# Performance work log

Measured on AMD Instinct MI355X. Metric: run time of the kernel, lower is better.

The kernel has to match this reference:

```python
import jax, jax.numpy as jnp
import numpy as np

EPS = 1e-5

def _bn(x, gamma, beta):
    # x: [B, N, C]; training-mode BatchNorm1d over (B, N)
    mu = jnp.mean(x, axis=(0, 1))
    var = jnp.var(x, axis=(0, 1))
    return (x - mu) * jax.lax.rsqrt(var + EPS) * gamma + beta


def setup_inputs() -> dict:
    key = jax.random.key(0)
    ks = jax.random.split(key, 32)
    B, N = 16, 8192
    enc_dim, mem_dim = 1024, 1024
    feat_dim = enc_dim + mem_dim  # 2048
    n_points = 2048
    s = 0.02
    d = {
        'partial': jax.random.normal(ks[0], (B, N, 3), jnp.float32),
        # first_conv: Conv1d(3,128,1) + BN(128) + ReLU + Conv1d(128,256,1)
        'W1': jax.random.normal(ks[1], (128, 3), jnp.float32) * s,
        'b1': jnp.zeros((128,), jnp.float32),
        'g1': jnp.ones((128,), jnp.float32),
        'be1': jnp.zeros((128,), jnp.float32),
        'W2': jax.random.normal(ks[2], (256, 128), jnp.float32) * s,
        'b2': jnp.zeros((256,), jnp.float32),
        # second_conv: Conv1d(512,512,1) + BN(512) + ReLU + Conv1d(512,enc_dim,1)
        'W3': jax.random.normal(ks[3], (512, 512), jnp.float32) * s,
        'b3': jnp.zeros((512,), jnp.float32),
        'g2': jnp.ones((512,), jnp.float32),
        'be2': jnp.zeros((512,), jnp.float32),
        'W4': jax.random.normal(ks[4], (enc_dim, 512), jnp.float32) * s,
        'b4': jnp.zeros((enc_dim,), jnp.float32),
        # MemoryModule gates: Linear(enc_dim, mem_dim) x4 + memory param
        'Wf': jax.random.normal(ks[5], (mem_dim, enc_dim), jnp.float32) * s,
        'bf': jnp.zeros((mem_dim,), jnp.float32),
        'Wi': jax.random.normal(ks[6], (mem_dim, enc_dim), jnp.float32) * s,
        'bi': jnp.zeros((mem_dim,), jnp.float32),
        'Wo': jax.random.normal(ks[7], (mem_dim, enc_dim), jnp.float32) * s,
        'bo': jnp.zeros((mem_dim,), jnp.float32),
        'Wc': jax.random.normal(ks[8], (mem_dim, enc_dim), jnp.float32) * s,
        'bc': jnp.zeros((mem_dim,), jnp.float32),
        'mem': jax.random.normal(ks[9], (1, mem_dim), jnp.float32),
        # Decoder MLP: feat_dim->2048->2048->2048->3*n_points
        'D1w': jax.random.normal(ks[10], (2048, feat_dim), jnp.float32) * s,
        'D1b': jnp.zeros((2048,), jnp.float32),
        'D2w': jax.random.normal(ks[11], (2048, 2048), jnp.float32) * s,
        'D2b': jnp.zeros((2048,), jnp.float32),
        'D3w': jax.random.normal(ks[12], (2048, 2048), jnp.float32) * s,
        'D3b': jnp.zeros((2048,), jnp.float32),
        'D4w': jax.random.normal(ks[13], (3 * n_points, 2048), jnp.float32) * s,
        'D4b': jnp.zeros((3 * n_points,), jnp.float32),
    }
    return d


def reference(partial, W1, b1, g1, be1, W2, b2, W3, b3, g2, be2, W4, b4,
              Wf, bf, Wi, bi, Wo, bo, Wc, bc, mem,
              D1w, D1b, D2w, D2b, D3w, D3b, D4w, D4b):
    B, N, _ = partial.shape
    # --- Encoder first_conv (pointwise convs == per-point linear) ---
    f = jnp.einsum('bnc,dc->bnd', partial, W1) + b1          # [B,N,128]
    f = jax.nn.relu(_bn(f, g1, be1))
    f = jnp.einsum('bnc,dc->bnd', f, W2) + b2                # [B,N,256]
    fg = jnp.max(f, axis=1, keepdims=True)                   # [B,1,256]
    f = jnp.concatenate([jnp.broadcast_to(fg, (B, N, 256)), f], axis=-1)  # [B,N,512]
    # --- second_conv ---
    f = jnp.einsum('bnc,dc->bnd', f, W3) + b3                # [B,N,512]
    f = jax.nn.relu(_bn(f, g2, be2))
    f = jnp.einsum('bnc,dc->bnd', f, W4) + b4                # [B,N,enc_dim]
    feat_global = jnp.max(f, axis=1)                         # [B,enc_dim]
    # --- MemoryModule (flag=False: memory not updated) ---
    fgate = jax.nn.sigmoid(feat_global @ Wf.T + bf)
    igate = jax.nn.sigmoid(feat_global @ Wi.T + bi)
    ogate = jax.nn.sigmoid(feat_global @ Wo.T + bo)
    cand = jnp.tanh(feat_global @ Wc.T + bc)
    mem_b = jnp.broadcast_to(mem, fgate.shape)
    h = ogate * jnp.tanh(fgate * mem_b + igate * cand)       # [B,mem_dim]
    feat = jnp.concatenate([feat_global, h], axis=1)         # [B,feat_dim]
    # --- Decoder MLP ---
    z = jax.nn.relu(feat @ D1w.T + D1b)
    z = jax.nn.relu(z @ D2w.T + D2b)
    z = jax.nn.relu(z @ D3w.T + D3b)
    z = z @ D4w.T + D4b                                      # [B, 3*n_points]
    return z.reshape(B, -1, 3)
```

## Files before the change

kernel.cpp:

```cpp
#include <hip/hip_runtime.h>
#include <hip/hip_bf16.h>

typedef __bf16 v8bf __attribute__((ext_vector_type(8)));
typedef float  v4f  __attribute__((ext_vector_type(4)));

#define NPTS (16*8192)
#define RPB  8192

__device__ __forceinline__ unsigned fenc(float x){
    unsigned u = __float_as_uint(x);
    return (u & 0x80000000u) ? ~u : (u | 0x80000000u);
}
__device__ __forceinline__ float fdec(unsigned u){
    return __uint_as_float((u & 0x80000000u) ? (u ^ 0x80000000u) : ~u);
}

__device__ __forceinline__ v8bf bn_relu8(v8bf v, float4 s0, float4 s1, float4 h0, float4 h1){
    v8bf r;
    r[0] = (__bf16)fmaxf(fmaf((float)v[0], s0.x, h0.x), 0.f);
    r[1] = (__bf16)fmaxf(fmaf((float)v[1], s0.y, h0.y), 0.f);
    r[2] = (__bf16)fmaxf(fmaf((float)v[2], s0.z, h0.z), 0.f);
    r[3] = (__bf16)fmaxf(fmaf((float)v[3], s0.w, h0.w), 0.f);
    r[4] = (__bf16)fmaxf(fmaf((float)v[4], s1.x, h1.x), 0.f);
    r[5] = (__bf16)fmaxf(fmaf((float)v[5], s1.y, h1.y), 0.f);
    r[6] = (__bf16)fmaxf(fmaf((float)v[6], s1.z, h1.z), 0.f);
    r[7] = (__bf16)fmaxf(fmaf((float)v[7], s1.w, h1.w), 0.f);
    return r;
}

__global__ __launch_bounds__(256) void stats1_k(const float* __restrict__ P,
        const float* __restrict__ W1, const float* __restrict__ b1,
        float* __restrict__ gsum, float* __restrict__ gsumsq)
{
    int tid = threadIdx.x;
    int c = tid & 127, half = tid >> 7;
    float w0 = W1[c*3+0], w1 = W1[c*3+1], w2 = W1[c*3+2], bb = b1[c];
    float s = 0.f, s2 = 0.f;
    int base = blockIdx.x * 512 + half;
    for (int i = 0; i < 256; ++i) {
        int p = base + i*2;
        float x = P[p*3+0], y = P[p*3+1], z = P[p*3+2];
        float v = fmaf(w0,x, fmaf(w1,y, fmaf(w2,z, bb)));
        s += v; s2 = fmaf(v,v,s2);
    }
    __shared__ float ls[256], lq[256];
    ls[tid] = s; lq[tid] = s2;
    __syncthreads();
    if (half == 0) {
        atomicAdd(&gsum[c],   s  + ls[tid+128]);
        atomicAdd(&gsumsq[c], s2 + lq[tid+128]);
    }
}

__global__ void finalize_k(const float* __restrict__ gsum, const float* __restrict__ gsumsq,
        const float* __restrict__ gamma, const float* __restrict__ beta,
        float* __restrict__ scale, float* __restrict__ shift, int C, float invn)
{
    int c = blockIdx.x*blockDim.x + threadIdx.x;
    if (c >= C) return;
    float m   = gsum[c]*invn;
    float var = fmaxf(gsumsq[c]*invn - m*m, 0.f);
    float rs  = rsqrtf(var + 1e-5f);
    float sc  = gamma[c]*rs;
    scale[c] = sc;
    shift[c] = beta[c] - m*sc;
}

__global__ __launch_bounds__(256) void apply1_k(const float* __restrict__ P,
        const float* __restrict__ W1, const float* __restrict__ b1,
        const float* __restrict__ sc, const float* __restrict__ sh,
        __bf16* __restrict__ out)
{
    int tid = threadIdx.x;
    int c = tid & 127, ph = tid >> 7;
    float w0 = W1[c*3+0], w1 = W1[c*3+1], w2 = W1[c*3+2], bb = b1[c];
    float a = sc[c], b_ = sh[c];
    int base = blockIdx.x * 16 + ph;
    #pragma unroll
    for (int i = 0; i < 8; ++i) {
        int p = base + i*2;
        float x = P[p*3+0], y = P[p*3+1], z = P[p*3+2];
        float v = fmaf(w0,x, fmaf(w1,y, fmaf(w2,z, bb)));
        v = fmaxf(fmaf(v, a, b_), 0.f);
        out[(size_t)p*128 + c] = (__bf16)v;
    }
}

__global__ void cvt_k(const float* __restrict__ src, __bf16* __restrict__ dst,
                      int rows, int cols, int sstride, int coff)
{
    int i = blockIdx.x*256 + threadIdx.x;
    if (i >= rows*cols) return;
    int r = i / cols, c = i - r*cols;
    dst[i] = (__bf16)src[(size_t)r*sstride + coff + c];
}

template<bool STORE, bool DOMAX, int LOGNB>
__global__ __launch_bounds__(256, 2) void gemm_k(
        const __bf16* __restrict__ A, const __bf16* __restrict__ Bw,
        int K, int Nw,
        const float* __restrict__ bias, int bias_bstride,
        __bf16* __restrict__ Cout, unsigned* __restrict__ maxenc)
{
    __shared__ __bf16 As[128*64];
    __shared__ __bf16 Bs[128*64];
    const int tid  = threadIdx.x;
    const int lane = tid & 63;
    const int wave = tid >> 6;
    const int wr = wave >> 1, wc = wave & 1;
    const int nwg   = (int)gridDim.x;
    const int chunk = nwg >> 3;
    const int bi    = (int)blockIdx.x;
    const int li    = (bi & 7) * chunk + (bi >> 3);
    const int m0    = (li >> LOGNB) * 128;
    const int n0    = (li & ((1 << LOGNB) - 1)) * 128;
    const int srow = tid >> 3, sslot = tid & 7;

    v4f acc[4][4];
    #pragma unroll
    for (int i=0;i<4;i++)
      #pragma unroll
      for (int j=0;j<4;j++) acc[i][j] = (v4f)(0.0f);

    v8bf ra[4], rb[4];
    #pragma unroll
    for (int i=0;i<4;i++){
        int r = i*32 + srow;
        ra[i] = *(const v8bf*)(A  + (size_t)(m0+r)*K + sslot*8);
        rb[i] = *(const v8bf*)(Bw + (size_t)(n0+r)*K + sslot*8);
    }

    for (int k0 = 0; k0 < K; k0 += 64) {
        __syncthreads();
        #pragma unroll
        for (int i=0;i<4;i++){
            int r = i*32 + srow;
            int p = sslot ^ (r & 7);
            *(v8bf*)(&As[r*64 + p*8]) = ra[i];
            *(v8bf*)(&Bs[r*64 + p*8]) = rb[i];
        }
        __syncthreads();
        if (k0 + 64 < K) {
            #pragma unroll
            for (int i=0;i<4;i++){
                int r = i*32 + srow;
                ra[i] = *(const v8bf*)(A  + (size_t)(m0+r)*K + (k0+64) + sslot*8);
                rb[i] = *(const v8bf*)(Bw + (size_t)(n0+r)*K + (k0+64) + sslot*8);
            }
        }
        #pragma unroll
        for (int kk = 0; kk < 2; ++kk) {
            v8bf af[4], bfr[4];
            #pragma unroll
            for (int i=0;i<4;i++){
                int arow = wr*64 + i*16 + (lane & 15);
                int slog = kk*4 + (lane >> 4);
                af[i]  = *(const v8bf*)(&As[arow*64 + ((slog ^ (arow & 7))<<3)]);
                int brow = wc*64 + i*16 + (lane & 15);
                bfr[i] = *(const v8bf*)(&Bs[brow*64 + ((slog ^ (brow & 7))<<3)]);
            }
            #pragma unroll
            for (int i=0;i<4;i++)
              #pragma unroll
              for (int j=0;j<4;j++)
                acc[i][j] = __builtin_amdgcn_mfma_f32_16x16x32_bf16(af[i], bfr[j], acc[i][j], 0,0,0);
        }
    }

    const int b = m0 / RPB;
    const float* brow_ = bias + (size_t)b * bias_bstride;
    float colmax[4];
    #pragma unroll
    for (int j=0;j<4;j++) colmax[j] = -3.402823466e38f;

    #pragma unroll
    for (int i=0;i<4;i++){
        int rbase = m0 + wr*64 + i*16 + ((lane>>4)<<2);
        #pragma unroll
        for (int j=0;j<4;j++){
            int col = n0 + wc*64 + j*16 + (lane & 15);
            float bv = brow_[col];
            #pragma unroll
            for (int q=0;q<4;q++){
                float v = acc[i][j][q] + bv;
                if constexpr (STORE) Cout[(size_t)(rbase+q)*Nw + col] = (__bf16)v;
                if constexpr (DOMAX) colmax[j] = fmaxf(colmax[j], v);
            }
        }
    }
    if constexpr (DOMAX) {
        #pragma unroll
        for (int j=0;j<4;j++){
            float v = colmax[j];
            v = fmaxf(v, __shfl_xor(v, 16));
            v = fmaxf(v, __shfl_xor(v, 32));
            if (lane < 16) {
                int col = n0 + wc*64 + j*16 + lane;
                atomicMax(&maxenc[(size_t)b*Nw + col], fenc(v));
            }
        }
    }
}

template<bool STORE, bool DOMAX, bool STATS, bool BNA, int LOGNB>
__global__ __launch_bounds__(512, 2) void gemm8_k(
        const __bf16* __restrict__ A, const __bf16* __restrict__ Bw,
        int K, int Nw,
        const float* __restrict__ bias, int bias_bstride,
        __bf16* __restrict__ Cout, unsigned* __restrict__ maxenc,
        float* __restrict__ gsum, float* __restrict__ gsq,
        const float* __restrict__ scA, const float* __restrict__ shA)
{
    __shared__ __bf16 lds[2][2][256*64];
    __shared__ float bnbuf[2][512];

    const int tid  = threadIdx.x;
    const int lane = tid & 63;
    const int wave = tid >> 6;
    const int wr = wave >> 2, wc = wave & 3;
    const int nwg   = (int)gridDim.x;
    const int chunk = nwg >> 3;
    const int bi    = (int)blockIdx.x;
    const int li    = (bi & 7) * chunk + (bi >> 3);
    const int m0    = (li >> LOGNB) * 256;
    const int n0    = (li & ((1 << LOGNB) - 1)) * 256;
    const int srow = tid >> 3;
    const int slot = tid & 7;

    if constexpr (BNA) {
        for (int c = tid; c < K; c += 512) {
            bnbuf[0][c] = scA[c];
            bnbuf[1][c] = shA[c];
        }
    }

    v4f acc[8][4];
    #pragma unroll
    for (int i=0;i<8;i++)
      #pragma unroll
      for (int j=0;j<4;j++) acc[i][j] = (v4f)(0.0f);

    v8bf ga[4], gb[4];
    auto issue = [&](int kb){
        #pragma unroll
        for (int p=0;p<4;p++){
            int r = p*64 + srow;
            ga[p] = *(const v8bf*)(A  + (size_t)(m0+r)*K + kb + slot*8);
            gb[p] = *(const v8bf*)(Bw + (size_t)(n0+r)*K + kb + slot*8);
        }
    };
    auto wr_lds = [&](int buf, int kb){
        float4 s0{}, s1{}, h0{}, h1{};
        if constexpr (BNA) {
            int kk = kb + slot*8;
            s0 = *(const float4*)&bnbuf[0][kk];
            s1 = *(const float4*)&bnbuf[0][kk+4];
            h0 = *(const float4*)&bnbuf[1][kk];
            h1 = *(const float4*)&bnbuf[1][kk+4];
        }
        #pragma unroll
        for (int p=0;p<4;p++){
            int r = p*64 + srow;
            int sl = slot ^ (r & 7);
            v8bf va = ga[p];
            if constexpr (BNA) va = bn_relu8(va, s0, s1, h0, h1);
            *(v8bf*)(&lds[buf][0][r*64 + sl*8]) = va;
            *(v8bf*)(&lds[buf][1][r*64 + sl*8]) = gb[p];
        }
    };

    if constexpr (BNA) __syncthreads();
    issue(0);
    wr_lds(0, 0);
    issue(64);
    __syncthreads();

    const int nt = K >> 6;
    for (int t = 0; t < nt; ++t) {
        const __bf16* as_ = &lds[t & 1][0][0];
        const __bf16* bs_ = &lds[t & 1][1][0];
        v8bf bfr[4][2];
        #pragma unroll
        for (int ph = 0; ph < 4; ++ph) {
            v8bf af[2][2];
            if (ph == 0) {
                #pragma unroll
                for (int nf=0;nf<4;nf++)
                  #pragma unroll
                  for (int kk=0;kk<2;kk++){
                    int brow = wc*64 + nf*16 + (lane & 15);
                    int sg = kk*4 + (lane >> 4);
                    bfr[nf][kk] = *(const v8bf*)(bs_ + brow*64 + ((sg ^ (brow & 7))<<3));
                  }
            }
            #pragma unroll
            for (int i=0;i<2;i++)
              #pragma unroll
              for (int kk=0;kk<2;kk++){
                int arow = wr*128 + (ph*2+i)*16 + (lane & 15);
                int sg = kk*4 + (lane >> 4);
                af[i][kk] = *(const v8bf*)(as_ + arow*64 + ((sg ^ (arow & 7))<<3));
              }
            __builtin_amdgcn_s_barrier();
            asm volatile("s_waitcnt lgkmcnt(0)" ::: "memory");
            __builtin_amdgcn_sched_barrier(0);
            __builtin_amdgcn_s_setprio(1);
            #pragma unroll
            for (int i=0;i<2;i++)
              #pragma unroll
              for (int nf=0;nf<4;nf++)
                acc[ph*2+i][nf] = __builtin_amdgcn_mfma_f32_16x16x32_bf16(af[i][0], bfr[nf][0], acc[ph*2+i][nf], 0,0,0);
            #pragma unroll
            for (int i=0;i<2;i++)
              #pragma unroll
              for (int nf=0;nf<4;nf++)
                acc[ph*2+i][nf] = __builtin_amdgcn_mfma_f32_16x16x32_bf16(af[i][1], bfr[nf][1], acc[ph*2+i][nf], 0,0,0);
            __builtin_amdgcn_s_setprio(0);
            if (ph < 3) {
                __builtin_amdgcn_s_barrier();
            } else {
                __syncthreads();
                if (t + 1 < nt) wr_lds((t+1) & 1, (t+1) << 6);
                if (t + 2 < nt) issue((t+2) << 6);
                __syncthreads();
            }
        }
    }

    const int b = m0 / RPB;
    const float* brow_ = bias + (size_t)b * bias_bstride;
    float colmax[4], csum[4], csq[4];
    #pragma unroll
    for (int j=0;j<4;j++){ colmax[j] = -3.402823466e38f; csum[j]=0.f; csq[j]=0.f; }

    #pragma unroll
    for (int i=0;i<8;i++){
        int rbase = m0 + wr*128 + i*16 + ((lane>>4)<<2);
        #pragma unroll
        for (int j=0;j<4;j++){
            int col = n0 + wc*64 + j*16 + (lane & 15);
            float bv = brow_[col];
            #pragma unroll
            for (int q=0;q<4;q++){
                float v = acc[i][j][q] + bv;
                if constexpr (STORE) Cout[(size_t)(rbase+q)*Nw + col] = (__bf16)v;
                if constexpr (DOMAX) colmax[j] = fmaxf(colmax[j], v);
                if constexpr (STATS) { csum[j] += v; csq[j] = fmaf(v,v,csq[j]); }
            }
        }
    }
    if constexpr (DOMAX) {
        #pragma unroll
        for (int j=0;j<4;j++){
            float v = colmax[j];
            v = fmaxf(v, __shfl_xor(v, 16));
            v = fmaxf(v, __shfl_xor(v, 32));
            if (lane < 16) {
                int col = n0 + wc*64 + j*16 + lane;
                atomicMax(&maxenc[(size_t)b*Nw + col], fenc(v));
            }
        }
    }
    if constexpr (STATS) {
        float* lst = (float*)&lds[0][0][0];
        #pragma unroll
        for (int j=0;j<4;j++){
            float s = csum[j], q = csq[j];
            s += __shfl_xor(s, 16); s += __shfl_xor(s, 32);
            q += __shfl_xor(q, 16); q += __shfl_xor(q, 32);
            if (lane < 16) {
                int c = wc*64 + j*16 + lane;
                lst[(wr*2+0)*256 + c] = s;
                lst[(wr*2+1)*256 + c] = q;
            }
        }
        __syncthreads();
        if (tid < 256) {
            float s = lst[0*256 + tid] + lst[2*256 + tid];
            float q = lst[1*256 + tid] + lst[3*256 + tid];
            atomicAdd(&gsum[n0 + tid], s);
            atomicAdd(&gsq [n0 + tid], q);
        }
    }
}

__global__ __launch_bounds__(256) void bias3_k(const unsigned* __restrict__ fge,
        const float* __restrict__ W3, const float* __restrict__ b3,
        float* __restrict__ bias3)
{
    int b = blockIdx.x, tid = threadIdx.x;
    __shared__ float fg[256];
    fg[tid] = fdec(fge[b*256 + tid]);
    __syncthreads();
    for (int d = tid; d < 512; d += 256) {
        const float* wrow = W3 + (size_t)d*512;
        float s = b3[d];
        for (int c = 0; c < 256; c += 4) {
            s = fmaf(fg[c+0], wrow[c+0], s);
            s = fmaf(fg[c+1], wrow[c+1], s);
            s = fmaf(fg[c+2], wrow[c+2], s);
            s = fmaf(fg[c+3], wrow[c+3], s);
        }
        bias3[b*512 + d] = s;
    }
}

__global__ void decode_k(const unsigned* __restrict__ enc, float* __restrict__ feat)
{
    int i = blockIdx.x*256 + threadIdx.x;
    int b = i >> 10, c = i & 1023;
    feat[(size_t)b*2048 + c] = fdec(enc[i]);
}

__global__ __launch_bounds__(256) void gates_k(
        const float* __restrict__ Wf, const float* __restrict__ bfv,
        const float* __restrict__ Wi, const float* __restrict__ biv,
        const float* __restrict__ Wo, const float* __restrict__ bov,
        const float* __restrict__ Wc, const float* __restrict__ bcv,
        const float* __restrict__ memv, float* __restrict__ feat)
{
    int tid = threadIdx.x;
    int b = tid & 15;
    int j = blockIdx.x*16 + (tid >> 4);
    const float* x  = feat + (size_t)b*2048;
    const float* rf = Wf + (size_t)j*1024;
    const float* ri = Wi + (size_t)j*1024;
    const float* ro = Wo + (size_t)j*1024;
    const float* rc = Wc + (size_t)j*1024;
    float sf = bfv[j], si = biv[j], so = bov[j], scn = bcv[j];
    for (int c = 0; c < 1024; c += 4) {
        float4 xv = *(const float4*)(x + c);
        float4 a  = *(const float4*)(rf + c);
        sf = fmaf(xv.x,a.x, fmaf(xv.y,a.y, fmaf(xv.z,a.z, fmaf(xv.w,a.w, sf))));
        float4 bq = *(const float4*)(ri + c);
        si = fmaf(xv.x,bq.x, fmaf(xv.y,bq.y, fmaf(xv.z,bq.z, fmaf(xv.w,bq.w, si))));
        float4 cq = *(const float4*)(ro + c);
        so = fmaf(xv.x,cq.x, fmaf(xv.y,cq.y, fmaf(xv.z,cq.z, fmaf(xv.w,cq.w, so))));
        float4 dq = *(const float4*)(rc + c);
        scn= fmaf(xv.x,dq.x, fmaf(xv.y,dq.y, fmaf(xv.z,dq.z, fmaf(xv.w,dq.w, scn))));
    }
    float fg = 1.f/(1.f + expf(-sf));
    float ig = 1.f/(1.f + expf(-si));
    float og = 1.f/(1.f + expf(-so));
    float cd = tanhf(scn);
    float h  = og * tanhf(fmaf(fg, memv[j], ig*cd));
    feat[(size_t)b*2048 + 1024 + j] = h;
}

template<bool RELU>
__global__ __launch_bounds__(256) void dec_k(const float* __restrict__ in,
        const float* __restrict__ W, const float* __restrict__ bias,
        float* __restrict__ out, int N)
{
    __shared__ float xin[2048];
    int tid = threadIdx.x;
    int b    = (blockIdx.x*4) / N;
    int col0 = (blockIdx.x*4) % N;
    for (int k = tid; k < 2048; k += 256) xin[k] = in[(size_t)b*2048 + k];
    __syncthreads();
    int lane = tid & 63;
    int col  = col0 + (tid >> 6);
    const float* wrow = W + (size_t)col*2048;
    float s = 0.f;
    for (int k = lane*4; k < 2048; k += 256) {
        float4 wv = *(const float4*)(wrow + k);
        float4 xv = *(const float4*)(&xin[k]);
        s = fmaf(wv.x,xv.x, fmaf(wv.y,xv.y, fmaf(wv.z,xv.z, fmaf(wv.w,xv.w, s))));
    }
    #pragma unroll
    for (int off = 32; off; off >>= 1) s += __shfl_xor(s, off);
    if (lane == 0) {
        s += bias[col];
        if (RELU) s = fmaxf(s, 0.f);
        out[(size_t)b*N + col] = s;
    }
}

extern "C" void kernel_launch(void* const* d_in, const int* in_sizes, int n_in,
                              void* d_out, int out_size, void* d_ws, size_t ws_size,
                              hipStream_t stream)
{
    (void)in_sizes; (void)n_in; (void)out_size; (void)ws_size;
    const float* partial = (const float*)d_in[0];
    const float* W1 = (const float*)d_in[1];
    const float* b1 = (const float*)d_in[2];
    const float* g1 = (const float*)d_in[3];
    const float* be1= (const float*)d_in[4];
    const float* W2 = (const float*)d_in[5];
    const float* b2 = (const float*)d_in[6];
    const float* W3 = (const float*)d_in[7];
    const float* b3 = (const float*)d_in[8];
    const float* g2 = (const float*)d_in[9];
    const float* be2= (const float*)d_in[10];
    const float* W4 = (const float*)d_in[11];
    const float* b4 = (const float*)d_in[12];
    const float* Wf = (const float*)d_in[13];
    const float* bfv= (const float*)d_in[14];
    const float* Wi = (const float*)d_in[15];
    const float* biv= (const float*)d_in[16];
    const float* Wo = (const float*)d_in[17];
    const float* bov= (const float*)d_in[18];
    const float* Wc = (const float*)d_in[19];
    const float* bcv= (const float*)d_in[20];
    const float* memv=(const float*)d_in[21];
    const float* D1w= (const float*)d_in[22];
    const float* D1b= (const float*)d_in[23];
    const float* D2w= (const float*)d_in[24];
    const float* D2b= (const float*)d_in[25];
    const float* D3w= (const float*)d_in[26];
    const float* D3b= (const float*)d_in[27];
    const float* D4w= (const float*)d_in[28];
    const float* D4b= (const float*)d_in[29];

    char* w = (char*)d_ws;
    size_t off = 0;
    auto alloc = [&](size_t bytes) -> void* {
        void* p = w + off; off += (bytes + 255) & ~(size_t)255; return p;
    };
    __bf16* y1bn = (__bf16*)alloc((size_t)NPTS*128*2);
    __bf16* f2   = (__bf16*)alloc((size_t)NPTS*256*2);
    __bf16* y3   = (__bf16*)alloc((size_t)NPTS*512*2);
    __bf16* W2b  = (__bf16*)alloc(256*128*2);
    __bf16* W3bb = (__bf16*)alloc(512*256*2);
    __bf16* W4b  = (__bf16*)alloc(1024*512*2);
    char* accbase = (char*)(w + off);
    float* gsum1    = (float*)alloc(128*4);
    float* gsumsq1  = (float*)alloc(128*4);
    float* gsum3    = (float*)alloc(512*4);
    float* gsumsq3  = (float*)alloc(512*4);
    unsigned* fg_enc    = (unsigned*)alloc(16*256*4);
    unsigned* featg_enc = (unsigned*)alloc(16*1024*4);
    size_t accbytes = (size_t)((w + off) - accbase);
    float* scale1 = (float*)alloc(128*4);
    float* shift1 = (float*)alloc(128*4);
    float* scale3 = (float*)alloc(512*4);
    float* shift3 = (float*)alloc(512*4);
    float* bias3  = (float*)alloc(16*512*4);
    float* feat   = (float*)alloc(16*2048*4);
    float* z1     = (float*)alloc(16*2048*4);
    float* z2     = (float*)alloc(16*2048*4);
    float* z3     = (float*)alloc(16*2048*4);

    hipMemsetAsync(accbase, 0, accbytes, stream);

    cvt_k<<<dim3(128), 256, 0, stream>>>(W2, W2b, 256, 128, 128, 0);
    cvt_k<<<dim3(512), 256, 0, stream>>>(W3, W3bb, 512, 256, 512, 256);
    cvt_k<<<dim3(2048),256, 0, stream>>>(W4, W4b, 1024, 512, 512, 0);

    stats1_k<<<dim3(256), 256, 0, stream>>>(partial, W1, b1, gsum1, gsumsq1);
    finalize_k<<<dim3(1), 128, 0, stream>>>(gsum1, gsumsq1, g1, be1, scale1, shift1, 128, 1.f/NPTS);
    apply1_k<<<dim3(8192), 256, 0, stream>>>(partial, W1, b1, scale1, shift1, y1bn);

    gemm_k<true,true,1><<<dim3(2048), 256, 0, stream>>>(
        y1bn, W2b, 128, 256, b2, 0, f2, fg_enc);

    bias3_k<<<dim3(16), 256, 0, stream>>>(fg_enc, W3, b3, bias3);

    gemm8_k<true,false,true,false,1><<<dim3(1024), 512, 0, stream>>>(
        f2, W3bb, 256, 512, bias3, 512, y3, nullptr, gsum3, gsumsq3, nullptr, nullptr);

    finalize_k<<<dim3(2), 256, 0, stream>>>(gsum3, gsumsq3, g2, be2, scale3, shift3, 512, 1.f/NPTS);

    gemm8_k<false,true,false,true,2><<<dim3(2048), 512, 0, stream>>>(
        y3, W4b, 512, 1024, b4, 0, nullptr, featg_enc, nullptr, nullptr, scale3, shift3);

    decode_k<<<dim3(64), 256, 0, stream>>>(featg_enc, feat);
    gates_k<<<dim3(64), 256, 0, stream>>>(Wf,bfv, Wi,biv, Wo,bov, Wc,bcv, memv, feat);

    dec_k<true ><<<dim3(8192),  256, 0, stream>>>(feat, D1w, D1b, z1, 2048);
    dec_k<true ><<<dim3(8192),  256, 0, stream>>>(z1,   D2w, D2b, z2, 2048);
    dec_k<true ><<<dim3(8192),  256, 0, stream>>>(z2,   D3w, D3b, z3, 2048);
    dec_k<false><<<dim3(24576), 256, 0, stream>>>(z3,   D4w, D4b, (float*)d_out, 6144);
}
```

Measured before the change: 574.2 us.

## Shrink GEMM M-tile with simpler single-buffer loop and batch decoder across all rows

The large-tile GEMM kernel is replaced by one using 128x256 tiles, a single LDS buffer with register prefetch, and BN+ReLU applied to A directly from global scale and shift arrays. Grid sizes double to match the smaller tile. The decoder GEMV kernel now keeps all 16 batch rows in LDS, so each weight row is read once instead of 16 times. This cuts decoder weight traffic sharply. The GEMM loses its double buffering and explicit MFMA scheduling, which may hurt its throughput.

```diff
diff --git a/kernel.cpp b/kernel.cpp
--- a/kernel.cpp
+++ b/kernel.cpp
@@ -203,7 +203,7 @@
 }
 
 template<bool STORE, bool DOMAX, bool STATS, bool BNA, int LOGNB>
-__global__ __launch_bounds__(512, 2) void gemm8_k(
+__global__ __launch_bounds__(512, 2) void gemmw_k(
         const __bf16* __restrict__ A, const __bf16* __restrict__ Bw,
         int K, int Nw,
         const float* __restrict__ bias, int bias_bstride,
@@ -211,9 +211,9 @@
         float* __restrict__ gsum, float* __restrict__ gsq,
         const float* __restrict__ scA, const float* __restrict__ shA)
 {
-    __shared__ __bf16 lds[2][2][256*64];
-    __shared__ float bnbuf[2][512];
-
+    __shared__ __bf16 As[128*64];
+    __shared__ __bf16 Bs[256*64];
+    __shared__ float lstat[2][2][256];
     const int tid  = threadIdx.x;
     const int lane = tid & 63;
     const int wave = tid >> 6;
@@ -222,108 +222,75 @@
     const int chunk = nwg >> 3;
     const int bi    = (int)blockIdx.x;
     const int li    = (bi & 7) * chunk + (bi >> 3);
-    const int m0    = (li >> LOGNB) * 256;
+    const int m0    = (li >> LOGNB) * 128;
     const int n0    = (li & ((1 << LOGNB) - 1)) * 256;
     const int srow = tid >> 3;
     const int slot = tid & 7;
 
-    if constexpr (BNA) {
-        for (int c = tid; c < K; c += 512) {
-            bnbuf[0][c] = scA[c];
-            bnbuf[1][c] = shA[c];
-        }
-    }
-
-    v4f acc[8][4];
-    #pragma unroll
-    for (int i=0;i<8;i++)
+    v4f acc[4][4];
+    #pragma unroll
+    for (int i=0;i<4;i++)
       #pragma unroll
       for (int j=0;j<4;j++) acc[i][j] = (v4f)(0.0f);
 
-    v8bf ga[4], gb[4];
-    auto issue = [&](int kb){
-        #pragma unroll
-        for (int p=0;p<4;p++){
-            int r = p*64 + srow;
-            ga[p] = *(const v8bf*)(A  + (size_t)(m0+r)*K + kb + slot*8);
-            gb[p] = *(const v8bf*)(Bw + (size_t)(n0+r)*K + kb + slot*8);
-        }
-    };
-    auto wr_lds = [&](int buf, int kb){
+    v8bf ra[2], rb[4];
+    auto loadAB = [&](int kb){
         float4 s0{}, s1{}, h0{}, h1{};
         if constexpr (BNA) {
             int kk = kb + slot*8;
-            s0 = *(const float4*)&bnbuf[0][kk];
-            s1 = *(const float4*)&bnbuf[0][kk+4];
-            h0 = *(const float4*)&bnbuf[1][kk];
-            h1 = *(const float4*)&bnbuf[1][kk+4];
-        }
-        #pragma unroll
-        for (int p=0;p<4;p++){
-            int r = p*64 + srow;
-            int sl = slot ^ (r & 7);
-            v8bf va = ga[p];
-            if constexpr (BNA) va = bn_relu8(va, s0, s1, h0, h1);
-            *(v8bf*)(&lds[buf][0][r*64 + sl*8]) = va;
-            *(v8bf*)(&lds[buf][1][r*64 + sl*8]) = gb[p];
+            s0 = *(const float4*)(scA + kk);
+            s1 = *(const float4*)(scA + kk + 4);
+            h0 = *(const float4*)(shA + kk);
+            h1 = *(const float4*)(shA + kk + 4);
+        }
+        #pragma unroll
+        for (int i=0;i<2;i++){
+            int r = i*64 + srow;
+            v8bf v = *(const v8bf*)(A + (size_t)(m0+r)*K + kb + slot*8);
+            if constexpr (BNA) v = bn_relu8(v, s0, s1, h0, h1);
+            ra[i] = v;
+        }
+        #pragma unroll
+        for (int i=0;i<4;i++){
+            int r = i*64 + srow;
+            rb[i] = *(const v8bf*)(Bw + (size_t)(n0+r)*K + kb + slot*8);
         }
     };
 
-    if constexpr (BNA) __syncthreads();
-    issue(0);
-    wr_lds(0, 0);
-    issue(64);
-    __syncthreads();
-
-    const int nt = K >> 6;
-    for (int t = 0; t < nt; ++t) {
-        const __bf16* as_ = &lds[t & 1][0][0];
-        const __bf16* bs_ = &lds[t & 1][1][0];
-        v8bf bfr[4][2];
-        #pragma unroll
-        for (int ph = 0; ph < 4; ++ph) {
-            v8bf af[2][2];
-            if (ph == 0) {
-                #pragma unroll
-                for (int nf=0;nf<4;nf++)
-                  #pragma unroll
-                  for (int kk=0;kk<2;kk++){
-                    int brow = wc*64 + nf*16 + (lane & 15);
-                    int sg = kk*4 + (lane >> 4);
-                    bfr[nf][kk] = *(const v8bf*)(bs_ + brow*64 + ((sg ^ (brow & 7))<<3));
-                  }
-            }
-            #pragma unroll
-            for (int i=0;i<2;i++)
+    loadAB(0);
+
+    for (int k0 = 0; k0 < K; k0 += 64) {
+        __syncthreads();
+        #pragma unroll
+        for (int i=0;i<2;i++){
+            int r = i*64 + srow;
+            int p = slot ^ (r & 7);
+            *(v8bf*)(&As[r*64 + p*8]) = ra[i];
+        }
+        #pragma unroll
+        for (int i=0;i<4;i++){
+            int r = i*64 + srow;
+            int p = slot ^ (r & 7);
+            *(v8bf*)(&Bs[r*64 + p*8]) = rb[i];
+        }
+        __syncthreads();
+        if (k0 + 64 < K) loadAB(k0 + 64);
+        #pragma unroll
+        for (int kk = 0; kk < 2; ++kk) {
+            v8bf af[4], bfr[4];
+            #pragma unroll
+            for (int i=0;i<4;i++){
+                int arow = wr*64 + i*16 + (lane & 15);
+                int sg = kk*4 + (lane >> 4);
+                af[i]  = *(const v8bf*)(&As[arow*64 + ((sg ^ (arow & 7))<<3)]);
+                int brow = wc*64 + i*16 + (lane & 15);
+                bfr[i] = *(const v8bf*)(&Bs[brow*64 + ((sg ^ (brow & 7))<<3)]);
+            }
+            #pragma unroll
+            for (int i=0;i<4;i++)
               #pragma unroll
-              for (int kk=0;kk<2;kk++){
-                int arow = wr*128 + (ph*2+i)*16 + (lane & 15);
-                int sg = kk*4 + (lane >> 4);
-                af[i][kk] = *(const v8bf*)(as_ + arow*64 + ((sg ^ (arow & 7))<<3));
-              }
-            __builtin_amdgcn_s_barrier();
-            asm volatile("s_waitcnt lgkmcnt(0)" ::: "memory");
-            __builtin_amdgcn_sched_barrier(0);
-            __builtin_amdgcn_s_setprio(1);
-            #pragma unroll
-            for (int i=0;i<2;i++)
-              #pragma unroll
-              for (int nf=0;nf<4;nf++)
-                acc[ph*2+i][nf] = __builtin_amdgcn_mfma_f32_16x16x32_bf16(af[i][0], bfr[nf][0], acc[ph*2+i][nf], 0,0,0);
-            #pragma unroll
-            for (int i=0;i<2;i++)
-              #pragma unroll
-              for (int nf=0;nf<4;nf++)
-                acc[ph*2+i][nf] = __builtin_amdgcn_mfma_f32_16x16x32_bf16(af[i][1], bfr[nf][1], acc[ph*2+i][nf], 0,0,0);
-            __builtin_amdgcn_s_setprio(0);
-            if (ph < 3) {
-                __builtin_amdgcn_s_barrier();
-            } else {
-                __syncthreads();
-                if (t + 1 < nt) wr_lds((t+1) & 1, (t+1) << 6);
-                if (t + 2 < nt) issue((t+2) << 6);
-                __syncthreads();
-            }
+              for (int j=0;j<4;j++)
+                acc[i][j] = __builtin_amdgcn_mfma_f32_16x16x32_bf16(af[i], bfr[j], acc[i][j], 0,0,0);
         }
     }
 
@@ -334,8 +301,8 @@
     for (int j=0;j<4;j++){ colmax[j] = -3.402823466e38f; csum[j]=0.f; csq[j]=0.f; }
 
     #pragma unroll
-    for (int i=0;i<8;i++){
-        int rbase = m0 + wr*128 + i*16 + ((lane>>4)<<2);
+    for (int i=0;i<4;i++){
+        int rbase = m0 + wr*64 + i*16 + ((lane>>4)<<2);
         #pragma unroll
         for (int j=0;j<4;j++){
             int col = n0 + wc*64 + j*16 + (lane & 15);
@@ -362,7 +329,6 @@
         }
     }
     if constexpr (STATS) {
-        float* lst = (float*)&lds[0][0][0];
         #pragma unroll
         for (int j=0;j<4;j++){
             float s = csum[j], q = csq[j];
@@ -370,14 +336,14 @@
             q += __shfl_xor(q, 16); q += __shfl_xor(q, 32);
             if (lane < 16) {
                 int c = wc*64 + j*16 + lane;
-                lst[(wr*2+0)*256 + c] = s;
-                lst[(wr*2+1)*256 + c] = q;
+                lstat[0][wr][c] = s;
+                lstat[1][wr][c] = q;
             }
         }
         __syncthreads();
         if (tid < 256) {
-            float s = lst[0*256 + tid] + lst[2*256 + tid];
-            float q = lst[1*256 + tid] + lst[3*256 + tid];
+            float s = lstat[0][0][tid] + lstat[0][1][tid];
+            float q = lstat[1][0][tid] + lstat[1][1][tid];
             atomicAdd(&gsum[n0 + tid], s);
             atomicAdd(&gsq [n0 + tid], q);
         }
@@ -448,31 +414,47 @@
 }
 
 template<bool RELU>
-__global__ __launch_bounds__(256) void dec_k(const float* __restrict__ in,
+__global__ __launch_bounds__(256) void dec2_k(const float* __restrict__ in,
         const float* __restrict__ W, const float* __restrict__ bias,
         float* __restrict__ out, int N)
 {
-    __shared__ float xin[2048];
+    __shared__ float xin[16*2048];
     int tid = threadIdx.x;
-    int b    = (blockIdx.x*4) / N;
-    int col0 = (blockIdx.x*4) % N;
-    for (int k = tid; k < 2048; k += 256) xin[k] = in[(size_t)b*2048 + k];
+    for (int i = tid; i < 8192; i += 256)
+        *(float4*)&xin[i*4] = *(const float4*)&in[i*4];
     __syncthreads();
-    int lane = tid & 63;
-    int col  = col0 + (tid >> 6);
-    const float* wrow = W + (size_t)col*2048;
-    float s = 0.f;
-    for (int k = lane*4; k < 2048; k += 256) {
-        float4 wv = *(const float4*)(wrow + k);
-        float4 xv = *(const float4*)(&xin[k]);
-        s = fmaf(wv.x,xv.x, fmaf(wv.y,xv.y, fmaf(wv.z,xv.z, fmaf(wv.w,xv.w, s))));
-    }
-    #pragma unroll
-    for (int off = 32; off; off >>= 1) s += __shfl_xor(s, off);
-    if (lane == 0) {
-        s += bias[col];
-        if (RELU) s = fmaxf(s, 0.f);
-        out[(size_t)b*N + col] = s;
+    int lane = tid & 63, wv = tid >> 6;
+    #pragma unroll
+    for (int c = 0; c < 2; ++c) {
+        int col = blockIdx.x*8 + wv*2 + c;
+        const float* wrow = W + (size_t)col*2048;
+        float s[16];
+        #pragma unroll
+        for (int b=0;b<16;b++) s[b]=0.f;
+        #pragma unroll
+        for (int it = 0; it < 8; ++it) {
+            int k = it*256 + lane*4;
+            float4 w4 = *(const float4*)(wrow + k);
+            #pragma unroll
+            for (int b=0;b<16;b++){
+                const float* xb = &xin[b*2048 + k];
+                s[b] = fmaf(w4.x, xb[0], fmaf(w4.y, xb[1], fmaf(w4.z, xb[2], fmaf(w4.w, xb[3], s[b]))));
+            }
+        }
+        #pragma unroll
+        for (int off=32; off; off>>=1){
+            #pragma unroll
+            for (int b=0;b<16;b++) s[b] += __shfl_xor(s[b], off);
+        }
+        if (lane == 0) {
+            float bv = bias[col];
+            #pragma unroll
+            for (int b=0;b<16;b++){
+                float v = s[b] + bv;
+                if (RELU) v = fmaxf(v, 0.f);
+                out[(size_t)b*N + col] = v;
+            }
+        }
     }
 }
 
@@ -556,19 +538,19 @@
 
     bias3_k<<<dim3(16), 256, 0, stream>>>(fg_enc, W3, b3, bias3);
 
-    gemm8_k<true,false,true,false,1><<<dim3(1024), 512, 0, stream>>>(
+    gemmw_k<true,false,true,false,1><<<dim3(2048), 512, 0, stream>>>(
         f2, W3bb, 256, 512, bias3, 512, y3, nullptr, gsum3, gsumsq3, nullptr, nullptr);
 
     finalize_k<<<dim3(2), 256, 0, stream>>>(gsum3, gsumsq3, g2, be2, scale3, shift3, 512, 1.f/NPTS);
 
-    gemm8_k<false,true,false,true,2><<<dim3(2048), 512, 0, stream>>>(
+    gemmw_k<false,true,false,true,2><<<dim3(4096), 512, 0, stream>>>(
         y3, W4b, 512, 1024, b4, 0, nullptr, featg_enc, nullptr, nullptr, scale3, shift3);
 
     decode_k<<<dim3(64), 256, 0, stream>>>(featg_enc, feat);
     gates_k<<<dim3(64), 256, 0, stream>>>(Wf,bfv, Wi,biv, Wo,bov, Wc,bcv, memv, feat);
 
-    dec_k<true ><<<dim3(8192),  256, 0, stream>>>(feat, D1w, D1b, z1, 2048);
-    dec_k<true ><<<dim3(8192),  256, 0, stream>>>(z1,   D2w, D2b, z2, 2048);
-    dec_k<true ><<<dim3(8192),  256, 0, stream>>>(z2,   D3w, D3b, z3, 2048);
-    dec_k<false><<<dim3(24576), 256, 0, stream>>>(z3,   D4w, D4b, (float*)d_out, 6144);
-}
+    dec2_k<true ><<<dim3(256), 256, 0, stream>>>(feat, D1w, D1b, z1, 2048);
+    dec2_k<true ><<<dim3(256), 256, 0, stream>>>(z1,   D2w, D2b, z2, 2048);
+    dec2_k<true ><<<dim3(256), 256, 0, stream>>>(z2,   D3w, D3b, z3, 2048);
+    dec2_k<false><<<dim3(768), 256, 0, stream>>>(z3,   D4w, D4b, (float*)d_out, 6144);
+}
```

Measured after the change: 603.3 us. +5.1%, slower.
